# Performance work log

Hardware: AMD Instinct MI355X
Metric: run time of the kernel (lower is better)

Reference implementation:

```python
import jax, jax.numpy as jnp
import numpy as np

B, N, K = 4, 8192, 16
D_POINTS, D_MODEL, INIT_DIM = 64, 64, 3

def _lin(key, din, dout, bias=True):
    k1, k2 = jax.random.split(key)
    s = 1.0 / np.sqrt(din)
    w = jax.random.uniform(k1, (din, dout), minval=-s, maxval=s, dtype=jnp.float32)
    if not bias:
        return w
    b = jax.random.uniform(k2, (dout,), minval=-s, maxval=s, dtype=jnp.float32)
    return w, b

def setup_inputs() -> dict:
    key = jax.random.key(0)
    ks = jax.random.split(key, 12)
    xyz = jax.random.normal(ks[0], (B, N, INIT_DIM), dtype=jnp.float32)
    features = jax.random.normal(ks[1], (B, N, D_POINTS), dtype=jnp.float32)
    knn_idx = jax.random.randint(ks[2], (B, N, K), 0, N)
    fc1_w, fc1_b = _lin(ks[3], D_POINTS, D_MODEL)
    fc2_w, fc2_b = _lin(ks[4], D_MODEL, D_POINTS)
    d1_w, d1_b = _lin(ks[5], INIT_DIM, D_MODEL)
    d2_w, d2_b = _lin(ks[6], D_MODEL, D_MODEL)
    g1_w, g1_b = _lin(ks[7], D_MODEL, D_MODEL)
    g2_w, g2_b = _lin(ks[8], D_MODEL, D_MODEL)
    wq = _lin(ks[9], D_MODEL, D_MODEL, bias=False)
    wk = _lin(ks[10], D_MODEL, D_MODEL, bias=False)
    wv = _lin(ks[11], D_MODEL, D_MODEL, bias=False)
    return dict(xyz=xyz, features=features, knn_idx=knn_idx,
                fc1_w=fc1_w, fc1_b=fc1_b, fc2_w=fc2_w, fc2_b=fc2_b,
                d1_w=d1_w, d1_b=d1_b, d2_w=d2_w, d2_b=d2_b,
                g1_w=g1_w, g1_b=g1_b, g2_w=g2_w, g2_b=g2_b,
                wq=wq, wk=wk, wv=wv)

def _index_points(x, idx):
    # x: (B, N, D), idx: (B, M, K) -> (B, M, K, D)
    return jax.vmap(lambda xb, ib: xb[ib])(x, idx)

def reference(xyz, features, knn_idx,
              fc1_w, fc1_b, fc2_w, fc2_b,
              d1_w, d1_b, d2_w, d2_b,
              g1_w, g1_b, g2_w, g2_b,
              wq, wk, wv):
    idx = knn_idx[:, :, :K]
    knn_xyz = _index_points(xyz, idx)                      # (B,N,K,3)
    pre = features
    x = features @ fc1_w + fc1_b                           # (B,N,d_model)
    q = x @ wq                                             # (B,N,d_model)
    k = _index_points(x @ wk, idx)                         # (B,N,K,d_model)
    v = _index_points(x @ wv, idx)                         # (B,N,K,d_model)
    rel = xyz[:, :, None, :] - knn_xyz                     # (B,N,K,3)
    pos_enc = jax.nn.relu(rel @ d1_w + d1_b) @ d2_w + d2_b # (B,N,K,d_model)
    h = q[:, :, None, :] - k + pos_enc
    attn = jax.nn.relu(h @ g1_w + g1_b) @ g2_w + g2_b      # (B,N,K,d_model)
    attn = jax.nn.softmax(attn / np.sqrt(D_MODEL), axis=-2)
    res = jnp.einsum('bmnf,bmnf->bmf', attn, v + pos_enc)  # (B,N,d_model)
    res = res @ fc2_w + fc2_b + pre                        # (B,N,d_points)
    return res, attn
```

## Files before the change

kernel.cpp:

```cpp
#include <hip/hip_runtime.h>
#include <hip/hip_bf16.h>

#define B_    4
#define N_    8192
#define TOT   (B_*N_)
#define KNN_  16
#define PPW   8
#define PITCH 80

typedef _Float16 half8  __attribute__((ext_vector_type(8)));
typedef float    floatx4 __attribute__((ext_vector_type(4)));

#define MFMA16(A, Bv, C) __builtin_amdgcn_mfma_f32_16x16x32_f16((A), (Bv), (C), 0, 0, 0)

__device__ __forceinline__ void lds_fence(){
  asm volatile("s_waitcnt lgkmcnt(0)" ::: "memory");
}
__device__ __forceinline__ half8 h8_load_f32(const float* __restrict__ p){
  float4 a = *(const float4*)p;
  float4 b = *(const float4*)(p + 4);
  half8 r;
  r[0] = (_Float16)a.x; r[1] = (_Float16)a.y; r[2] = (_Float16)a.z; r[3] = (_Float16)a.w;
  r[4] = (_Float16)b.x; r[5] = (_Float16)b.y; r[6] = (_Float16)b.z; r[7] = (_Float16)b.w;
  return r;
}
__device__ __forceinline__ void store8f(float* __restrict__ p, half8 v){
  float4 a = {(float)v[0], (float)v[1], (float)v[2], (float)v[3]};
  float4 b = {(float)v[4], (float)v[5], (float)v[6], (float)v[7]};
  *(float4*)p = a;
  *(float4*)(p + 4) = b;
}

__device__ void fill_w64(half8* dst, const float* __restrict__ W, int tid){
  for (int i = tid; i < 512; i += 256){
    int lane = i & 63, nt = (i >> 6) & 3, kt = i >> 8;
    int n  = nt*16 + (lane & 15);
    int kb = kt*32 + ((lane >> 4) & 3)*8;
    half8 v;
    #pragma unroll
    for (int j = 0; j < 8; j++) v[j] = (_Float16)W[(kb + j)*64 + n];
    dst[i] = v;
  }
}
__device__ void fill_d1(half8* dst, const float* __restrict__ W, int tid){
  if (tid < 256){
    int lane = tid & 63, nt = tid >> 6;
    int n  = nt*16 + (lane & 15);
    int kb = ((lane >> 4) & 3)*8;
    half8 v;
    #pragma unroll
    for (int j = 0; j < 8; j++){
      int k = kb + j;
      v[j] = (k < 3) ? (_Float16)W[k*64 + n] : (_Float16)0.0f;
    }
    dst[tid] = v;
  }
}

__global__ __launch_bounds__(256, 2) void k1_qkv(
    const float* __restrict__ feat, const float* __restrict__ fc1w, const float* __restrict__ fc1b,
    const float* __restrict__ wqw, const float* __restrict__ wkw, const float* __restrict__ wvw,
    _Float16* __restrict__ qws, _Float16* __restrict__ kws, _Float16* __restrict__ vws)
{
  __shared__ half8 Sfc1[512], Sq[512], Sk[512], Sv[512];
  __shared__ alignas(16) _Float16 xt[4][16*PITCH];
  const int tid = threadIdx.x;
  fill_w64(Sfc1, fc1w, tid);
  fill_w64(Sq, wqw, tid);
  fill_w64(Sk, wkw, tid);
  fill_w64(Sv, wvw, tid);
  __syncthreads();

  const int wave = tid >> 6, lane = tid & 63, quad = lane >> 4, m16 = lane & 15;
  _Float16* tx = &xt[wave][0];
  const int rowbase = blockIdx.x*64 + wave*16;
  float fb[4];
  #pragma unroll
  for (int nt = 0; nt < 4; nt++) fb[nt] = fc1b[nt*16 + m16];

  const int arow = rowbase + m16;
  half8 Fa0 = h8_load_f32(&feat[arow*64 + quad*8]);
  half8 Fa1 = h8_load_f32(&feat[arow*64 + 32 + quad*8]);
  const floatx4 z4 = {0.f, 0.f, 0.f, 0.f};

  #pragma unroll
  for (int nt = 0; nt < 4; nt++){
    floatx4 acc = MFMA16(Fa0, Sfc1[nt*64 + lane], z4);
    acc = MFMA16(Fa1, Sfc1[(4 + nt)*64 + lane], acc);
    const int col = nt*16 + m16;
    #pragma unroll
    for (int r = 0; r < 4; r++)
      tx[(quad*4 + r)*PITCH + col] = (_Float16)(acc[r] + fb[nt]);
  }
  lds_fence();
  const half8 Ax0 = *(const half8*)&tx[m16*PITCH + quad*8];
  const half8 Ax1 = *(const half8*)&tx[m16*PITCH + 32 + quad*8];

#define EMIT_QKV(S, OUT)                                                      \
  { _Pragma("unroll")                                                         \
    for (int nt = 0; nt < 4; nt++){                                           \
      floatx4 acc = MFMA16(Ax0, S[nt*64 + lane], z4);                         \
      acc = MFMA16(Ax1, S[(4 + nt)*64 + lane], acc);                          \
      _Pragma("unroll")                                                       \
      for (int r = 0; r < 4; r++)                                             \
        OUT[(rowbase + quad*4 + r)*64 + nt*16 + m16] = (_Float16)acc[r];      \
    } }
  EMIT_QKV(Sq, qws)
  EMIT_QKV(Sk, kws)
  EMIT_QKV(Sv, vws)
#undef EMIT_QKV
}

__global__ __launch_bounds__(256, 2) void k2_point(
    const float* __restrict__ xyz, const int* __restrict__ knn,
    const float* __restrict__ d1w, const float* __restrict__ d1b,
    const float* __restrict__ d2w, const float* __restrict__ d2b,
    const float* __restrict__ g1w, const float* __restrict__ g1b,
    const float* __restrict__ g2w, const float* __restrict__ g2b,
    const _Float16* __restrict__ qws, const _Float16* __restrict__ kws,
    const _Float16* __restrict__ vws,
    _Float16* __restrict__ r0, float* __restrict__ attn_out)
{
  __shared__ half8 Sd1[256], Sd2[512], Sg1[512], Sg2[512];
  __shared__ alignas(16) _Float16 tiles[4][2][16*PITCH];
  const int tid = threadIdx.x;
  fill_d1(Sd1, d1w, tid);
  fill_w64(Sd2, d2w, tid);
  fill_w64(Sg1, g1w, tid);
  fill_w64(Sg2, g2w, tid);
  __syncthreads();

  const int wave = tid >> 6, lane = tid & 63, quad = lane >> 4, m16 = lane & 15;
  _Float16* tA = &tiles[wave][0][0];
  _Float16* tB = &tiles[wave][1][0];

  half8 Fd1[4], Fd2[2][4], Fg1[2][4], Fg2[2][4];
  #pragma unroll
  for (int nt = 0; nt < 4; nt++){
    Fd1[nt] = Sd1[nt*64 + lane];
    #pragma unroll
    for (int kt = 0; kt < 2; kt++){
      Fd2[kt][nt] = Sd2[(kt*4 + nt)*64 + lane];
      Fg1[kt][nt] = Sg1[(kt*4 + nt)*64 + lane];
      Fg2[kt][nt] = Sg2[(kt*4 + nt)*64 + lane];
    }
  }
  float bd1[4], bd2[4], bg1[4], bg2[4];
  #pragma unroll
  for (int nt = 0; nt < 4; nt++){
    const int c = nt*16 + m16;
    bd1[nt] = d1b[c]; bd2[nt] = d2b[c];
    bg1[nt] = g1b[c]; bg2[nt] = g2b[c];
  }
  const floatx4 z4 = {0.f, 0.f, 0.f, 0.f};

  for (int p = 0; p < PPW; p++){
    const int gpt  = blockIdx.x*(4*PPW) + wave*PPW + p;
    const int b    = gpt >> 13;
    const int idxm = knn[gpt*KNN_ + m16];
    const int grow = b*N_ + idxm;

    half8 Ar;
    #pragma unroll
    for (int j = 0; j < 8; j++) Ar[j] = (_Float16)0.0f;
    if (quad == 0){
      #pragma unroll
      for (int j = 0; j < 3; j++)
        Ar[j] = (_Float16)(xyz[gpt*3 + j] - xyz[grow*3 + j]);
    }

    #pragma unroll
    for (int nt = 0; nt < 4; nt++){
      floatx4 acc = MFMA16(Ar, Fd1[nt], z4);
      const int col = nt*16 + m16;
      #pragma unroll
      for (int r = 0; r < 4; r++){
        float t = acc[r] + bd1[nt];
        tA[(quad*4 + r)*PITCH + col] = (_Float16)(t > 0.f ? t : 0.f);
      }
    }
    lds_fence();
    const half8 At0 = *(const half8*)&tA[m16*PITCH + quad*8];
    const half8 At1 = *(const half8*)&tA[m16*PITCH + 32 + quad*8];

    #pragma unroll
    for (int nt = 0; nt < 4; nt++){
      floatx4 acc = MFMA16(At0, Fd2[0][nt], z4);
      acc = MFMA16(At1, Fd2[1][nt], acc);
      const int col = nt*16 + m16;
      #pragma unroll
      for (int r = 0; r < 4; r++)
        tB[(quad*4 + r)*PITCH + col] = (_Float16)(acc[r] + bd2[nt]);
    }
    lds_fence();
    const half8 Pa0 = *(const half8*)&tB[m16*PITCH + quad*8];
    const half8 Pa1 = *(const half8*)&tB[m16*PITCH + 32 + quad*8];

    const half8 Ka0 = *(const half8*)&kws[grow*64 + quad*8];
    const half8 Ka1 = *(const half8*)&kws[grow*64 + 32 + quad*8];
    const half8 Qa0 = *(const half8*)&qws[gpt*64 + quad*8];
    const half8 Qa1 = *(const half8*)&qws[gpt*64 + 32 + quad*8];
    const half8 H0 = Qa0 - Ka0 + Pa0;
    const half8 H1 = Qa1 - Ka1 + Pa1;

    #pragma unroll
    for (int nt = 0; nt < 4; nt++){
      floatx4 acc = MFMA16(H0, Fg1[0][nt], z4);
      acc = MFMA16(H1, Fg1[1][nt], acc);
      const int col = nt*16 + m16;
      #pragma unroll
      for (int r = 0; r < 4; r++){
        float t = acc[r] + bg1[nt];
        tA[(quad*4 + r)*PITCH + col] = (_Float16)(t > 0.f ? t : 0.f);
      }
    }
    lds_fence();
    const half8 U0 = *(const half8*)&tA[m16*PITCH + quad*8];
    const half8 U1 = *(const half8*)&tA[m16*PITCH + 32 + quad*8];

    float A2[4][4];
    #pragma unroll
    for (int nt = 0; nt < 4; nt++){
      floatx4 acc = MFMA16(U0, Fg2[0][nt], z4);
      acc = MFMA16(U1, Fg2[1][nt], acc);
      #pragma unroll
      for (int r = 0; r < 4; r++) A2[nt][r] = acc[r] + bg2[nt];
    }

    #pragma unroll
    for (int nt = 0; nt < 4; nt++){
      float mx = fmaxf(fmaxf(A2[nt][0], A2[nt][1]), fmaxf(A2[nt][2], A2[nt][3]));
      mx = fmaxf(mx, __shfl_xor(mx, 16));
      mx = fmaxf(mx, __shfl_xor(mx, 32));
      float s = 0.f;
      #pragma unroll
      for (int r = 0; r < 4; r++){
        float e = expf((A2[nt][r] - mx)*0.125f);
        A2[nt][r] = e; s += e;
      }
      s += __shfl_xor(s, 16);
      s += __shfl_xor(s, 32);
      const float inv = 1.0f / s;
      const int col = nt*16 + m16;
      #pragma unroll
      for (int r = 0; r < 4; r++)
        tA[(quad*4 + r)*PITCH + col] = (_Float16)(A2[nt][r]*inv);
    }
    lds_fence();
    const half8 Aa0 = *(const half8*)&tA[m16*PITCH + quad*8];
    const half8 Aa1 = *(const half8*)&tA[m16*PITCH + 32 + quad*8];
    const half8 Va0 = *(const half8*)&vws[grow*64 + quad*8];
    const half8 Va1 = *(const half8*)&vws[grow*64 + 32 + quad*8];

    float* ap = attn_out + ((size_t)gpt*KNN_ + m16)*64;
    store8f(ap + quad*8, Aa0);
    store8f(ap + 32 + quad*8, Aa1);

    float w0[8], w1[8];
    #pragma unroll
    for (int j = 0; j < 8; j++){
      w0[j] = (float)Aa0[j] * ((float)Va0[j] + (float)Pa0[j]);
      w1[j] = (float)Aa1[j] * ((float)Va1[j] + (float)Pa1[j]);
    }
    #pragma unroll
    for (int mask = 1; mask < 16; mask <<= 1){
      #pragma unroll
      for (int j = 0; j < 8; j++){
        w0[j] += __shfl_xor(w0[j], mask);
        w1[j] += __shfl_xor(w1[j], mask);
      }
    }
    if (m16 == 0){
      half8 o0, o1;
      #pragma unroll
      for (int j = 0; j < 8; j++){ o0[j] = (_Float16)w0[j]; o1[j] = (_Float16)w1[j]; }
      *(half8*)&r0[gpt*64 + quad*8] = o0;
      *(half8*)&r0[gpt*64 + 32 + quad*8] = o1;
    }
  }
}

__global__ __launch_bounds__(256, 2) void k3_fc2(
    const _Float16* __restrict__ r0, const float* __restrict__ fc2w,
    const float* __restrict__ fc2b, const float* __restrict__ feat,
    float* __restrict__ out_res)
{
  __shared__ half8 S[512];
  const int tid = threadIdx.x;
  fill_w64(S, fc2w, tid);
  __syncthreads();

  const int wave = tid >> 6, lane = tid & 63, quad = lane >> 4, m16 = lane & 15;
  const int rowbase = blockIdx.x*64 + wave*16;
  float fb[4];
  #pragma unroll
  for (int nt = 0; nt < 4; nt++) fb[nt] = fc2b[nt*16 + m16];

  const half8 A0 = *(const half8*)&r0[(rowbase + m16)*64 + quad*8];
  const half8 A1 = *(const half8*)&r0[(rowbase + m16)*64 + 32 + quad*8];
  const floatx4 z4 = {0.f, 0.f, 0.f, 0.f};

  #pragma unroll
  for (int nt = 0; nt < 4; nt++){
    floatx4 acc = MFMA16(A0, S[nt*64 + lane], z4);
    acc = MFMA16(A1, S[(4 + nt)*64 + lane], acc);
    #pragma unroll
    for (int r = 0; r < 4; r++){
      const int rowg = rowbase + quad*4 + r;
      const int col  = nt*16 + m16;
      out_res[rowg*64 + col] = acc[r] + fb[nt] + feat[rowg*64 + col];
    }
  }
}

extern "C" void kernel_launch(void* const* d_in, const int* in_sizes, int n_in,
                              void* d_out, int out_size, void* d_ws, size_t ws_size,
                              hipStream_t stream)
{
  (void)in_sizes; (void)n_in; (void)out_size; (void)ws_size;
  const float* xyz  = (const float*)d_in[0];
  const float* feat = (const float*)d_in[1];
  const int*   knn  = (const int*)d_in[2];
  const float* fc1w = (const float*)d_in[3];
  const float* fc1b = (const float*)d_in[4];
  const float* fc2w = (const float*)d_in[5];
  const float* fc2b = (const float*)d_in[6];
  const float* d1w  = (const float*)d_in[7];
  const float* d1b  = (const float*)d_in[8];
  const float* d2w  = (const float*)d_in[9];
  const float* d2b  = (const float*)d_in[10];
  const float* g1w  = (const float*)d_in[11];
  const float* g1b  = (const float*)d_in[12];
  const float* g2w  = (const float*)d_in[13];
  const float* g2b  = (const float*)d_in[14];
  const float* wq   = (const float*)d_in[15];
  const float* wk   = (const float*)d_in[16];
  const float* wv   = (const float*)d_in[17];

  _Float16* ws  = (_Float16*)d_ws;
  _Float16* qws = ws;
  _Float16* kws = ws + (size_t)TOT*64;
  _Float16* vws = ws + (size_t)2*TOT*64;
  _Float16* r0  = ws + (size_t)3*TOT*64;

  float* out      = (float*)d_out;
  float* out_res  = out;
  float* out_attn = out + (size_t)TOT*64;

  k1_qkv<<<TOT/64, 256, 0, stream>>>(feat, fc1w, fc1b, wq, wk, wv, qws, kws, vws);
  k2_point<<<TOT/(4*PPW), 256, 0, stream>>>(xyz, knn, d1w, d1b, d2w, d2b,
                                            g1w, g1b, g2w, g2b,
                                            qws, kws, vws, r0, out_attn);
  k3_fc2<<<TOT/64, 256, 0, stream>>>(r0, fc2w, fc2b, feat, out_res);
}
```

Baseline: 268.7 us.

## Compute pos-enc first layer in scalar FMAs and reduce attention directly from MFMA registers

Replaces the 3-input d1 MFMA and its LDS round trip with per-lane scalar FMAs that build the A operand directly from float weights held in LDS. The softmax output is no longer staged through LDS. Attention is stored straight from the MFMA accumulator layout with nontemporal stores, and the weighted V sum uses per-row V gathers with two cross-quad shuffles instead of a 16-step butterfly. It also adds an XOR swizzle on the LDS tiles to avoid bank conflicts, prefetches the next point's knn index, uses exp2/rcp intrinsics, and raises the occupancy hint to 3 blocks. The cost is scattered 2-byte V gathers and higher register pressure under the tighter launch bounds.

```diff
diff --git a/kernel.cpp b/kernel.cpp
--- a/kernel.cpp
+++ b/kernel.cpp
@@ -24,12 +24,6 @@
   r[4] = (_Float16)b.x; r[5] = (_Float16)b.y; r[6] = (_Float16)b.z; r[7] = (_Float16)b.w;
   return r;
 }
-__device__ __forceinline__ void store8f(float* __restrict__ p, half8 v){
-  float4 a = {(float)v[0], (float)v[1], (float)v[2], (float)v[3]};
-  float4 b = {(float)v[4], (float)v[5], (float)v[6], (float)v[7]};
-  *(float4*)p = a;
-  *(float4*)(p + 4) = b;
-}
 
 __device__ void fill_w64(half8* dst, const float* __restrict__ W, int tid){
   for (int i = tid; i < 512; i += 256){
@@ -42,22 +36,8 @@
     dst[i] = v;
   }
 }
-__device__ void fill_d1(half8* dst, const float* __restrict__ W, int tid){
-  if (tid < 256){
-    int lane = tid & 63, nt = tid >> 6;
-    int n  = nt*16 + (lane & 15);
-    int kb = ((lane >> 4) & 3)*8;
-    half8 v;
-    #pragma unroll
-    for (int j = 0; j < 8; j++){
-      int k = kb + j;
-      v[j] = (k < 3) ? (_Float16)W[k*64 + n] : (_Float16)0.0f;
-    }
-    dst[tid] = v;
-  }
-}
-
-__global__ __launch_bounds__(256, 2) void k1_qkv(
+
+__global__ __launch_bounds__(256, 3) void k1_qkv(
     const float* __restrict__ feat, const float* __restrict__ fc1w, const float* __restrict__ fc1b,
     const float* __restrict__ wqw, const float* __restrict__ wkw, const float* __restrict__ wvw,
     _Float16* __restrict__ qws, _Float16* __restrict__ kws, _Float16* __restrict__ vws)
@@ -111,7 +91,7 @@
 #undef EMIT_QKV
 }
 
-__global__ __launch_bounds__(256, 2) void k2_point(
+__global__ __launch_bounds__(256, 3) void k2_point(
     const float* __restrict__ xyz, const int* __restrict__ knn,
     const float* __restrict__ d1w, const float* __restrict__ d1b,
     const float* __restrict__ d2w, const float* __restrict__ d2b,
@@ -121,23 +101,24 @@
     const _Float16* __restrict__ vws,
     _Float16* __restrict__ r0, float* __restrict__ attn_out)
 {
-  __shared__ half8 Sd1[256], Sd2[512], Sg1[512], Sg2[512];
+  __shared__ half8 Sd2[512], Sg1[512], Sg2[512];
+  __shared__ float4 Td1[64];
   __shared__ alignas(16) _Float16 tiles[4][2][16*PITCH];
   const int tid = threadIdx.x;
-  fill_d1(Sd1, d1w, tid);
   fill_w64(Sd2, d2w, tid);
   fill_w64(Sg1, g1w, tid);
   fill_w64(Sg2, g2w, tid);
+  if (tid < 64)
+    Td1[tid] = make_float4(d1w[tid], d1w[64 + tid], d1w[128 + tid], d1b[tid]);
   __syncthreads();
 
   const int wave = tid >> 6, lane = tid & 63, quad = lane >> 4, m16 = lane & 15;
   _Float16* tA = &tiles[wave][0][0];
   _Float16* tB = &tiles[wave][1][0];
 
-  half8 Fd1[4], Fd2[2][4], Fg1[2][4], Fg2[2][4];
+  half8 Fd2[2][4], Fg1[2][4], Fg2[2][4];
   #pragma unroll
   for (int nt = 0; nt < 4; nt++){
-    Fd1[nt] = Sd1[nt*64 + lane];
     #pragma unroll
     for (int kt = 0; kt < 2; kt++){
       Fd2[kt][nt] = Sd2[(kt*4 + nt)*64 + lane];
@@ -145,78 +126,92 @@
       Fg2[kt][nt] = Sg2[(kt*4 + nt)*64 + lane];
     }
   }
-  float bd1[4], bd2[4], bg1[4], bg2[4];
+  float bd2[4], bg1[4], bg2[4];
   #pragma unroll
   for (int nt = 0; nt < 4; nt++){
     const int c = nt*16 + m16;
-    bd1[nt] = d1b[c]; bd2[nt] = d2b[c];
-    bg1[nt] = g1b[c]; bg2[nt] = g2b[c];
+    bd2[nt] = d2b[c]; bg1[nt] = g1b[c]; bg2[nt] = g2b[c];
   }
   const floatx4 z4 = {0.f, 0.f, 0.f, 0.f};
+  const int wsw = quad << 3;
+  const int swz = (quad ^ (m16 >> 2)) << 3;
+
+  const int gpt0 = blockIdx.x*(4*PPW) + wave*PPW;
+  const int b    = gpt0 >> 13;
+  int grow_n = b*N_ + knn[gpt0*KNN_ + m16];
 
   for (int p = 0; p < PPW; p++){
-    const int gpt  = blockIdx.x*(4*PPW) + wave*PPW + p;
-    const int b    = gpt >> 13;
-    const int idxm = knn[gpt*KNN_ + m16];
-    const int grow = b*N_ + idxm;
-
-    half8 Ar;
-    #pragma unroll
-    for (int j = 0; j < 8; j++) Ar[j] = (_Float16)0.0f;
-    if (quad == 0){
-      #pragma unroll
-      for (int j = 0; j < 3; j++)
-        Ar[j] = (_Float16)(xyz[gpt*3 + j] - xyz[grow*3 + j]);
-    }
-
-    #pragma unroll
-    for (int nt = 0; nt < 4; nt++){
-      floatx4 acc = MFMA16(Ar, Fd1[nt], z4);
-      const int col = nt*16 + m16;
-      #pragma unroll
-      for (int r = 0; r < 4; r++){
-        float t = acc[r] + bd1[nt];
-        tA[(quad*4 + r)*PITCH + col] = (_Float16)(t > 0.f ? t : 0.f);
-      }
-    }
-    lds_fence();
-    const half8 At0 = *(const half8*)&tA[m16*PITCH + quad*8];
-    const half8 At1 = *(const half8*)&tA[m16*PITCH + 32 + quad*8];
-
-    #pragma unroll
-    for (int nt = 0; nt < 4; nt++){
-      floatx4 acc = MFMA16(At0, Fd2[0][nt], z4);
-      acc = MFMA16(At1, Fd2[1][nt], acc);
-      const int col = nt*16 + m16;
-      #pragma unroll
-      for (int r = 0; r < 4; r++)
-        tB[(quad*4 + r)*PITCH + col] = (_Float16)(acc[r] + bd2[nt]);
-    }
-    lds_fence();
-    const half8 Pa0 = *(const half8*)&tB[m16*PITCH + quad*8];
-    const half8 Pa1 = *(const half8*)&tB[m16*PITCH + 32 + quad*8];
+    const int gpt  = gpt0 + p;
+    const int grow = grow_n;
 
     const half8 Ka0 = *(const half8*)&kws[grow*64 + quad*8];
     const half8 Ka1 = *(const half8*)&kws[grow*64 + 32 + quad*8];
     const half8 Qa0 = *(const half8*)&qws[gpt*64 + quad*8];
     const half8 Qa1 = *(const half8*)&qws[gpt*64 + 32 + quad*8];
+    const float dx = xyz[gpt*3 + 0] - xyz[grow*3 + 0];
+    const float dy = xyz[gpt*3 + 1] - xyz[grow*3 + 1];
+    const float dz = xyz[gpt*3 + 2] - xyz[grow*3 + 2];
+
+    const int g0 = __shfl(grow, quad*4 + 0);
+    const int g1 = __shfl(grow, quad*4 + 1);
+    const int g2 = __shfl(grow, quad*4 + 2);
+    const int g3 = __shfl(grow, quad*4 + 3);
+
+    if (p < PPW-1) grow_n = b*N_ + knn[(gpt+1)*KNN_ + m16];
+
+    half8 At0, At1;
+    #pragma unroll
+    for (int j = 0; j < 8; j++){
+      const float4 w  = Td1[quad*8 + j];
+      const float4 w2 = Td1[32 + quad*8 + j];
+      float t  = fmaf(dx, w.x,  fmaf(dy, w.y,  fmaf(dz, w.z,  w.w)));
+      float t2 = fmaf(dx, w2.x, fmaf(dy, w2.y, fmaf(dz, w2.z, w2.w)));
+      At0[j] = (_Float16)(t  > 0.f ? t  : 0.f);
+      At1[j] = (_Float16)(t2 > 0.f ? t2 : 0.f);
+    }
+
+    float Pc[4][4];
+    #pragma unroll
+    for (int nt = 0; nt < 4; nt++){
+      floatx4 acc = MFMA16(At0, Fd2[0][nt], z4);
+      acc = MFMA16(At1, Fd2[1][nt], acc);
+      const int colS = (nt*16 + m16) ^ wsw;
+      #pragma unroll
+      for (int r = 0; r < 4; r++){
+        Pc[nt][r] = acc[r] + bd2[nt];
+        tB[(quad*4 + r)*PITCH + colS] = (_Float16)Pc[nt][r];
+      }
+    }
+    lds_fence();
+    const half8 Pa0 = *(const half8*)&tB[m16*PITCH + swz];
+    const half8 Pa1 = *(const half8*)&tB[m16*PITCH + 32 + swz];
     const half8 H0 = Qa0 - Ka0 + Pa0;
     const half8 H1 = Qa1 - Ka1 + Pa1;
 
+    _Float16 vg0[4], vg1[4], vg2[4], vg3[4];
+    #pragma unroll
+    for (int nt = 0; nt < 4; nt++){
+      const int c = nt*16 + m16;
+      vg0[nt] = vws[g0*64 + c];
+      vg1[nt] = vws[g1*64 + c];
+      vg2[nt] = vws[g2*64 + c];
+      vg3[nt] = vws[g3*64 + c];
+    }
+
     #pragma unroll
     for (int nt = 0; nt < 4; nt++){
       floatx4 acc = MFMA16(H0, Fg1[0][nt], z4);
       acc = MFMA16(H1, Fg1[1][nt], acc);
-      const int col = nt*16 + m16;
+      const int colS = (nt*16 + m16) ^ wsw;
       #pragma unroll
       for (int r = 0; r < 4; r++){
         float t = acc[r] + bg1[nt];
-        tA[(quad*4 + r)*PITCH + col] = (_Float16)(t > 0.f ? t : 0.f);
+        tA[(quad*4 + r)*PITCH + colS] = (_Float16)(t > 0.f ? t : 0.f);
       }
     }
     lds_fence();
-    const half8 U0 = *(const half8*)&tA[m16*PITCH + quad*8];
-    const half8 U1 = *(const half8*)&tA[m16*PITCH + 32 + quad*8];
+    const half8 U0 = *(const half8*)&tA[m16*PITCH + swz];
+    const half8 U1 = *(const half8*)&tA[m16*PITCH + 32 + swz];
 
     float A2[4][4];
     #pragma unroll
@@ -235,48 +230,36 @@
       float s = 0.f;
       #pragma unroll
       for (int r = 0; r < 4; r++){
-        float e = expf((A2[nt][r] - mx)*0.125f);
+        float e = exp2f((A2[nt][r] - mx)*0.18033688011112042f);
         A2[nt][r] = e; s += e;
       }
       s += __shfl_xor(s, 16);
       s += __shfl_xor(s, 32);
-      const float inv = 1.0f / s;
-      const int col = nt*16 + m16;
-      #pragma unroll
-      for (int r = 0; r < 4; r++)
-        tA[(quad*4 + r)*PITCH + col] = (_Float16)(A2[nt][r]*inv);
-    }
-    lds_fence();
-    const half8 Aa0 = *(const half8*)&tA[m16*PITCH + quad*8];
-    const half8 Aa1 = *(const half8*)&tA[m16*PITCH + 32 + quad*8];
-    const half8 Va0 = *(const half8*)&vws[grow*64 + quad*8];
-    const half8 Va1 = *(const half8*)&vws[grow*64 + 32 + quad*8];
-
-    float* ap = attn_out + ((size_t)gpt*KNN_ + m16)*64;
-    store8f(ap + quad*8, Aa0);
-    store8f(ap + 32 + quad*8, Aa1);
-
-    float w0[8], w1[8];
-    #pragma unroll
-    for (int j = 0; j < 8; j++){
-      w0[j] = (float)Aa0[j] * ((float)Va0[j] + (float)Pa0[j]);
-      w1[j] = (float)Aa1[j] * ((float)Va1[j] + (float)Pa1[j]);
-    }
-    #pragma unroll
-    for (int mask = 1; mask < 16; mask <<= 1){
-      #pragma unroll
-      for (int j = 0; j < 8; j++){
-        w0[j] += __shfl_xor(w0[j], mask);
-        w1[j] += __shfl_xor(w1[j], mask);
-      }
-    }
-    if (m16 == 0){
-      half8 o0, o1;
-      #pragma unroll
-      for (int j = 0; j < 8; j++){ o0[j] = (_Float16)w0[j]; o1[j] = (_Float16)w1[j]; }
-      *(half8*)&r0[gpt*64 + quad*8] = o0;
-      *(half8*)&r0[gpt*64 + 32 + quad*8] = o1;
-    }
+      const float inv = __builtin_amdgcn_rcpf(s);
+      #pragma unroll
+      for (int r = 0; r < 4; r++) A2[nt][r] *= inv;
+    }
+
+    float* ap = attn_out + (size_t)gpt*(KNN_*64);
+    float acc_s[4];
+    #pragma unroll
+    for (int nt = 0; nt < 4; nt++){
+      const int c = nt*16 + m16;
+      __builtin_nontemporal_store(A2[nt][0], &ap[(quad*4 + 0)*64 + c]);
+      __builtin_nontemporal_store(A2[nt][1], &ap[(quad*4 + 1)*64 + c]);
+      __builtin_nontemporal_store(A2[nt][2], &ap[(quad*4 + 2)*64 + c]);
+      __builtin_nontemporal_store(A2[nt][3], &ap[(quad*4 + 3)*64 + c]);
+      float ssum = A2[nt][0]*((float)vg0[nt] + Pc[nt][0])
+                 + A2[nt][1]*((float)vg1[nt] + Pc[nt][1])
+                 + A2[nt][2]*((float)vg2[nt] + Pc[nt][2])
+                 + A2[nt][3]*((float)vg3[nt] + Pc[nt][3]);
+      ssum += __shfl_xor(ssum, 16);
+      ssum += __shfl_xor(ssum, 32);
+      acc_s[nt] = ssum;
+    }
+    const float rv = (quad & 2) ? ((quad & 1) ? acc_s[3] : acc_s[2])
+                                : ((quad & 1) ? acc_s[1] : acc_s[0]);
+    r0[gpt*64 + quad*16 + m16] = (_Float16)rv;
   }
 }
 
```

Result: slower. 307.0 us (+14.3%).
